# Kernel optimization log

Measured on AMD Instinct MI355X. Metric: run time of the kernel, lower is better.

## Reference

```python
import jax, jax.numpy as jnp
import numpy as np

B, S, D_IN, D_OUT = 4, 2048, 1024, 1024
USE_MASK = True


def setup_inputs() -> dict:
    key = jax.random.key(0)
    ks = jax.random.split(key, 6)
    return {
        "inputs_for_keys": jax.random.normal(ks[0], (B, S, D_IN), jnp.float32),
        "inputs_for_values": jax.random.normal(ks[1], (B, S, D_IN), jnp.float32),
        "inputs_for_queries": jax.random.normal(ks[2], (B, S, D_IN), jnp.float32),
        "WK": jax.random.normal(ks[3], (D_IN, D_OUT), jnp.float32) * 0.1,
        "WV": jax.random.normal(ks[4], (D_IN, D_OUT), jnp.float32) * 0.1,
        "WQ": jax.random.normal(ks[5], (D_IN, D_OUT), jnp.float32) * 0.1,
    }


def reference(inputs_for_keys, inputs_for_values, inputs_for_queries, WK, WV, WQ):
    # projections: [B,S,Din] @ [Din,Dout] -> [B,S,Dout]
    K = jnp.einsum("bsd,de->bse", inputs_for_keys, WK)
    V = jnp.einsum("bsd,de->bse", inputs_for_values, WV)
    Q = jnp.einsum("bsd,de->bse", inputs_for_queries, WQ)

    dk = jnp.asarray(K.shape[2], jnp.float32)
    # scores: [B, Sq, Sk]
    score = jnp.einsum("bqd,bkd->bqk", Q, K) / jnp.sqrt(dk)
    if USE_MASK:
        # causal: -inf strictly above diagonal (j > i), matching the
        # transposed tril(-1) * -inf construction in the original.
        q_idx = jnp.arange(S)[:, None]
        k_idx = jnp.arange(S)[None, :]
        mask = jnp.where(k_idx > q_idx, -jnp.inf, 0.0).astype(score.dtype)
        score = score + mask[None, :, :]
    soft_score = jax.nn.softmax(score, axis=-1)
    return jnp.einsum("bqk,bkd->bqd", soft_score, V)
```

## Files before the change

### kernel.cpp

```cpp
#include <hip/hip_runtime.h>
#include <hip/hip_bf16.h>

typedef unsigned short u16;
typedef _Float16 f16;
typedef __attribute__((ext_vector_type(8))) short s16x8;
typedef __attribute__((ext_vector_type(8))) _Float16 f16x8;
typedef __attribute__((ext_vector_type(4))) float f32x4;
typedef __attribute__((ext_vector_type(4))) unsigned short u16x4;

template <typename T>
__device__ __forceinline__ auto mfma_try(T a, T b, f32x4 c, int)
    -> decltype(__builtin_amdgcn_mfma_f32_16x16x32_f16(a, b, c, 0, 0, 0)) {
  return __builtin_amdgcn_mfma_f32_16x16x32_f16(a, b, c, 0, 0, 0);
}
template <typename T>
__device__ __forceinline__ f32x4 mfma_try(T a, T b, f32x4 c, long) {
  return __builtin_amdgcn_mfma_f32_16x16x32_f16(
      __builtin_bit_cast(f16x8, a), __builtin_bit_cast(f16x8, b), c, 0, 0, 0);
}
__device__ __forceinline__ f32x4 MFMA16(s16x8 a, s16x8 b, f32x4 c) {
  return mfma_try(a, b, c, 0);
}

__device__ __forceinline__ void gload16(const void* g, void* s) {
  __builtin_amdgcn_global_load_lds(
      (const __attribute__((address_space(1))) void*)g,
      (__attribute__((address_space(3))) void*)s, 16, 0, 0);
}

__device__ __forceinline__ u16 f2h(float x) {
  f16 h = (f16)x;
  u16 u;
  __builtin_memcpy(&u, &h, 2);
  return u;
}
__device__ __forceinline__ float h2f(u16 u) {
  f16 h;
  __builtin_memcpy(&h, &u, 2);
  return (float)h;
}

#define LDS_SWZ(r, cb) ((cb) ^ (((r)&7) << 4))

__device__ __forceinline__ void bar() { __builtin_amdgcn_s_barrier(); }
__device__ __forceinline__ void lgkm0() {
  asm volatile("s_waitcnt lgkmcnt(0)" ::: "memory");
  __builtin_amdgcn_sched_barrier(0);
}
__device__ __forceinline__ void vm4() {
  asm volatile("s_waitcnt vmcnt(4)" ::: "memory");
}
__device__ __forceinline__ void vm0() {
  asm volatile("s_waitcnt vmcnt(0)" ::: "memory");
}

__device__ __forceinline__ void gemm256_core(
    const u16* __restrict__ Apan, int lda, const u16* __restrict__ Bpan,
    int ldb, int ns, char* lds, f32x4 (&acc)[8][4]) {
  const int tid = threadIdx.x;
  const int w = tid >> 6, l = tid & 63;
  const int wr = w >> 2, wc = w & 3;

  const int sr = tid >> 3;
  const int scol = (((tid & 7) * 16) ^ ((sr & 7) << 4)) >> 1;

  auto stageH = [&](const u16* pan, int ld, int t, int h, int region) {
    char* dst = lds + ((t & 1) << 16) + region * 16384 + (w << 10);
    const u16* src = pan + (long)(h * 128 + sr) * ld + t * 64 + scol;
    gload16(src, dst);
    gload16(src + (long)64 * ld, dst + 8192);
  };
  auto rdA = [&](int p, int m, int ks) -> s16x8 {
    int r = m * 16 + (l & 15);
    int cb = ks * 64 + ((l >> 4) << 4);
    return *(const s16x8*)(lds + (p << 16) + wr * 16384 + r * 128 + LDS_SWZ(r, cb));
  };
  auto rdB = [&](int p, int n, int ks) -> s16x8 {
    int row = wc * 64 + n * 16 + (l & 15);
    int r = row & 127;
    int cb = ks * 64 + ((l >> 4) << 4);
    return *(const s16x8*)(lds + (p << 16) + (2 + (wc >> 1)) * 16384 + r * 128 +
                           LDS_SWZ(r, cb));
  };

  stageH(Apan, lda, 0, 0, 0);
  stageH(Apan, lda, 0, 1, 1);
  stageH(Bpan, ldb, 0, 0, 2);
  stageH(Bpan, ldb, 0, 1, 3);
  if (ns > 1) {
    stageH(Apan, lda, 1, 0, 0);
    stageH(Apan, lda, 1, 1, 1);
    vm4();
  } else {
    vm0();
  }
  bar();

  for (int t = 0; t < ns; ++t) {
    const int p = t & 1;
    s16x8 af[8][2], bf[4][2];
    auto do_mfma = [&](int mb) {
#pragma unroll
      for (int m = 0; m < 2; ++m)
#pragma unroll
        for (int n = 0; n < 4; ++n) {
          acc[mb + m][n] = MFMA16(af[mb + m][0], bf[n][0], acc[mb + m][n]);
          acc[mb + m][n] = MFMA16(af[mb + m][1], bf[n][1], acc[mb + m][n]);
        }
    };
#pragma unroll
    for (int n = 0; n < 4; ++n) { bf[n][0] = rdB(p, n, 0); bf[n][1] = rdB(p, n, 1); }
#pragma unroll
    for (int m = 0; m < 2; ++m) { af[m][0] = rdA(p, m, 0); af[m][1] = rdA(p, m, 1); }
    if (t + 1 < ns) stageH(Bpan, ldb, t + 1, 0, 2);
    bar(); lgkm0();
    __builtin_amdgcn_s_setprio(1);
    do_mfma(0);
    __builtin_amdgcn_s_setprio(0);
    bar();
#pragma unroll
    for (int m = 2; m < 8; ++m) { af[m][0] = rdA(p, m, 0); af[m][1] = rdA(p, m, 1); }
    if (t + 1 < ns) stageH(Bpan, ldb, t + 1, 1, 3);
    bar(); lgkm0();
    __builtin_amdgcn_s_setprio(1);
    do_mfma(2);
    __builtin_amdgcn_s_setprio(0);
    bar();
    if (t + 2 < ns) stageH(Apan, lda, t + 2, 0, 0);
    bar(); lgkm0();
    __builtin_amdgcn_s_setprio(1);
    do_mfma(4);
    __builtin_amdgcn_s_setprio(0);
    bar();
    if (t + 2 < ns) stageH(Apan, lda, t + 2, 1, 1);
    bar(); lgkm0();
    __builtin_amdgcn_s_setprio(1);
    do_mfma(6);
    __builtin_amdgcn_s_setprio(0);
    if (t + 2 < ns) vm4(); else vm0();
    bar();
  }
}

__global__ __launch_bounds__(512, 2) void proj256_kernel(
    const u16* __restrict__ xk, const u16* __restrict__ xq, const u16* __restrict__ xv,
    const u16* __restrict__ wk, const u16* __restrict__ wq, const u16* __restrict__ wv,
    u16* __restrict__ K, u16* __restrict__ Q, u16* __restrict__ Vt) {
  __shared__ char lds[131072];
  const int y = blockIdx.y;
  const u16* X = y == 0 ? xk : (y == 1 ? xq : xv);
  const u16* W = y == 0 ? wk : (y == 1 ? wq : wv);
  const int bx = blockIdx.x;
  const int swz = (bx & 7) * 16 + (bx >> 3);
  const int tm = swz >> 2, tn = swz & 3;
  f32x4 acc[8][4] = {};
  gemm256_core(X + (long)tm * 256 * 1024, 1024, W + (long)tn * 256 * 1024, 1024,
               16, lds, acc);
  const int l = threadIdx.x & 63, w = threadIdx.x >> 6;
  const int wr = w >> 2, wc = w & 3;
  const int rg0 = tm * 256 + wr * 128, cg0 = tn * 256 + wc * 64;
  if (y < 2) {
    u16* C = y == 0 ? K : Q;
#pragma unroll
    for (int m = 0; m < 8; ++m)
#pragma unroll
      for (int n = 0; n < 4; ++n)
#pragma unroll
        for (int j = 0; j < 4; ++j) {
          int rg = rg0 + m * 16 + ((l >> 4) << 2) + j;
          int cg = cg0 + n * 16 + (l & 15);
          C[(long)rg * 1024 + cg] = f2h(acc[m][n][j]);
        }
  } else {
#pragma unroll
    for (int m = 0; m < 8; ++m) {
      int rg = rg0 + m * 16 + ((l >> 4) << 2);
      int b = rg >> 11, rl = rg & 2047;
#pragma unroll
      for (int n = 0; n < 4; ++n) {
        int cg = cg0 + n * 16 + (l & 15);
        u16x4 pk;
#pragma unroll
        for (int j = 0; j < 4; ++j) pk[j] = f2h(acc[m][n][j]);
        *(u16x4*)(Vt + (long)b * (1024 * 2048) + (long)cg * 2048 + rl) = pk;
      }
    }
  }
}

__global__ __launch_bounds__(512, 2) void qkt256_kernel(
    const u16* __restrict__ Q, const u16* __restrict__ K, u16* __restrict__ S) {
  __shared__ char lds[131072];
  const int bx = blockIdx.x;
  const int swz = (bx & 7) * 18 + (bx >> 3);
  const int b = swz / 36;
  int t = swz - b * 36;
  int tm = 0;
  while (t > tm) { t -= tm + 1; ++tm; }
  const int tn = t;
  f32x4 acc[8][4] = {};
  const u16* Qb = Q + (long)b * 2048 * 1024;
  const u16* Kb = K + (long)b * 2048 * 1024;
  gemm256_core(Qb + (long)tm * 256 * 1024, 1024, Kb + (long)tn * 256 * 1024,
               1024, 16, lds, acc);
  u16* Sb = S + (long)b * 2048 * 2048;
  const int l = threadIdx.x & 63, w = threadIdx.x >> 6;
  const int wr = w >> 2, wc = w & 3;
  const int rg0 = tm * 256 + wr * 128, cg0 = tn * 256 + wc * 64;
#pragma unroll
  for (int m = 0; m < 8; ++m)
#pragma unroll
    for (int n = 0; n < 4; ++n)
#pragma unroll
      for (int j = 0; j < 4; ++j) {
        int rg = rg0 + m * 16 + ((l >> 4) << 2) + j;
        int cg = cg0 + n * 16 + (l & 15);
        Sb[(long)rg * 2048 + cg] = f2h(acc[m][n][j]);
      }
}

struct Geom {
  int srow[4], scol[4];
  int w, l, wr, wc;
};

__device__ __forceinline__ Geom make_geom() {
  Geom g;
  int tid = threadIdx.x;
  g.w = tid >> 6; g.l = tid & 63;
  g.wr = g.w >> 1; g.wc = g.w & 1;
#pragma unroll
  for (int i = 0; i < 4; ++i) {
    int off = i * 4096 + g.w * 1024 + g.l * 16;
    int r = off >> 7, cb = off & 127;
    g.srow[i] = r;
    g.scol[i] = LDS_SWZ(r, cb) >> 1;
  }
  return g;
}

__device__ __forceinline__ void stage(const u16* pan, int ld, int k0,
                                      char* lds, const Geom& g) {
#pragma unroll
  for (int i = 0; i < 4; ++i)
    gload16(pan + (long)g.srow[i] * ld + k0 + g.scol[i],
            lds + i * 4096 + g.w * 1024);
}

__device__ __forceinline__ void compute_step(const char* lA, const char* lB,
                                             const Geom& g, f32x4 acc[4][4]) {
#pragma unroll
  for (int ks = 0; ks < 2; ++ks) {
    s16x8 af[4], bg[4];
#pragma unroll
    for (int m = 0; m < 4; ++m) {
      int r = g.wr * 64 + m * 16 + (g.l & 15);
      int cb = ks * 64 + ((g.l >> 4) << 4);
      af[m] = *(const s16x8*)(lA + r * 128 + LDS_SWZ(r, cb));
    }
#pragma unroll
    for (int n = 0; n < 4; ++n) {
      int r = g.wc * 64 + n * 16 + (g.l & 15);
      int cb = ks * 64 + ((g.l >> 4) << 4);
      bg[n] = *(const s16x8*)(lB + r * 128 + LDS_SWZ(r, cb));
    }
#pragma unroll
    for (int m = 0; m < 4; ++m)
#pragma unroll
      for (int n = 0; n < 4; ++n)
        acc[m][n] = MFMA16(af[m], bg[n], acc[m][n]);
  }
}

__device__ __forceinline__ void gemm_core(const u16* Apan, int lda,
                                          const u16* Bpan, int ldb, int nsteps,
                                          char* lA, char* lB, const Geom& g,
                                          f32x4 acc[4][4]) {
  stage(Apan, lda, 0, lA, g);
  stage(Bpan, ldb, 0, lB, g);
  __syncthreads();
  for (int t = 0; t < nsteps; ++t) {
    int cur = (t & 1) << 14;
    if (t + 1 < nsteps) {
      int nxt = ((t + 1) & 1) << 14;
      stage(Apan, lda, (t + 1) * 64, lA + nxt, g);
      stage(Bpan, ldb, (t + 1) * 64, lB + nxt, g);
    }
    compute_step(lA + cur, lB + cur, g, acc);
    if (t + 1 < nsteps) __syncthreads();
  }
}

__global__ __launch_bounds__(256, 2) void pv_kernel(
    const u16* __restrict__ P, const u16* __restrict__ Vt, float* __restrict__ O) {
  __shared__ char lds[65536];
  const int bx = blockIdx.x;
  const int swz = (bx & 7) * 64 + (bx >> 3);
  const int b = swz >> 7, loc = swz & 127;
  const int tm = loc >> 3, tn = loc & 7;
  Geom g = make_geom();
  f32x4 acc[4][4] = {};
  gemm_core(P + ((long)b * 2048 + tm * 128) * 2048, 2048,
            Vt + (long)b * 1024 * 2048 + (long)tn * 128 * 2048, 2048,
            (tm + 1) * 2, lds, lds + 32768, g, acc);
  const int rg0 = tm * 128 + g.wr * 64, cg0 = tn * 128 + g.wc * 64;
#pragma unroll
  for (int m = 0; m < 4; ++m)
#pragma unroll
    for (int n = 0; n < 4; ++n)
#pragma unroll
      for (int j = 0; j < 4; ++j) {
        int rg = rg0 + m * 16 + ((g.l >> 4) << 2) + j;
        int cg = cg0 + n * 16 + (g.l & 15);
        O[((long)b * 2048 + rg) * 1024 + cg] = acc[m][n][j];
      }
}

__global__ __launch_bounds__(256) void softmax_causal(
    const u16* __restrict__ S, u16* __restrict__ P) {
  const int row = blockIdx.x;
  const int i_q = row & 2047;
  const u16* sr = S + (long)row * 2048;
  u16* pr = P + (long)row * 2048;
  const int tid = threadIdx.x;
  const int l = tid & 63, w = tid >> 6;
  const int base = tid * 8;

  s16x8 raw = *(const s16x8*)(sr + base);
  float v[8];
  float m = -INFINITY;
#pragma unroll
  for (int j = 0; j < 8; ++j) {
    float x = h2f((u16)raw[j]);
    x = (base + j <= i_q) ? x : -INFINITY;
    v[j] = x;
    m = fmaxf(m, x);
  }
  __shared__ float red[8];
  for (int o = 32; o; o >>= 1) m = fmaxf(m, __shfl_xor(m, o, 64));
  if (l == 0) red[w] = m;
  __syncthreads();
  m = fmaxf(fmaxf(red[0], red[1]), fmaxf(red[2], red[3]));

  float s = 0.f;
#pragma unroll
  for (int j = 0; j < 8; ++j) {
    v[j] = expf(v[j] - m);
    s += v[j];
  }
  for (int o = 32; o; o >>= 1) s += __shfl_xor(s, o, 64);
  if (l == 0) red[4 + w] = s;
  __syncthreads();
  s = (red[4] + red[5]) + (red[6] + red[7]);
  float inv = 1.0f / s;

  s16x8 o;
#pragma unroll
  for (int j = 0; j < 8; ++j) o[j] = (short)f2h(v[j] * inv);
  *(s16x8*)(pr + base) = o;
}

__global__ __launch_bounds__(256) void xcast_kernel(
    const float* __restrict__ x0, const float* __restrict__ x1,
    const float* __restrict__ x2, u16* __restrict__ o0, u16* __restrict__ o1,
    u16* __restrict__ o2) {
  const int y = blockIdx.y;
  const float* in = y == 0 ? x0 : (y == 1 ? x1 : x2);
  u16* out = y == 0 ? o0 : (y == 1 ? o1 : o2);
  long i = ((long)blockIdx.x * 256 + threadIdx.x) * 8;
  f32x4 a = *(const f32x4*)(in + i);
  f32x4 b = *(const f32x4*)(in + i + 4);
  s16x8 o;
#pragma unroll
  for (int j = 0; j < 4; ++j) {
    o[j] = (short)f2h(a[j]);
    o[4 + j] = (short)f2h(b[j]);
  }
  *(s16x8*)(out + i) = o;
}

__global__ __launch_bounds__(256) void wcast_kernel(
    const float* __restrict__ wk, const float* __restrict__ wv,
    const float* __restrict__ wq, u16* __restrict__ ok, u16* __restrict__ ov,
    u16* __restrict__ oq) {
  __shared__ float tile[32][33];
  const int z = blockIdx.z;
  const float* w = z == 0 ? wk : (z == 1 ? wv : wq);
  u16* o = z == 0 ? ok : (z == 1 ? ov : oq);
  const float scale = (z == 2) ? 0.03125f : 1.0f;
  const int bx = blockIdx.x, by = blockIdx.y;
  const int lx = threadIdx.x & 31, ly = threadIdx.x >> 5;
#pragma unroll
  for (int j = 0; j < 32; j += 8)
    tile[ly + j][lx] = w[(long)(by * 32 + ly + j) * 1024 + bx * 32 + lx];
  __syncthreads();
#pragma unroll
  for (int j = 0; j < 32; j += 8)
    o[(long)(bx * 32 + ly + j) * 1024 + by * 32 + lx] = f2h(tile[lx][ly + j] * scale);
}

extern "C" void kernel_launch(void* const* d_in, const int* in_sizes, int n_in,
                              void* d_out, int out_size, void* d_ws, size_t ws_size,
                              hipStream_t stream) {
  const float* Xk = (const float*)d_in[0];
  const float* Xv = (const float*)d_in[1];
  const float* Xq = (const float*)d_in[2];
  const float* WK = (const float*)d_in[3];
  const float* WV = (const float*)d_in[4];
  const float* WQ = (const float*)d_in[5];

  const int Bn = 4, S = 2048, D = 1024;
  const long NX = (long)Bn * S * D;

  const size_t r0 = (size_t)Bn * S * S * 4;
  const size_t r1 = r0 + 3ull * D * D * 2;
  const size_t r2 = r1 + 2ull * NX * 2;
  const size_t NEED = r2 + (size_t)NX * 2;
  if (ws_size < NEED) {
    hipMemsetAsync(d_out, 0, (size_t)out_size * 4, stream);
    return;
  }
  char* ws = (char*)d_ws;
  u16* xkb = (u16*)ws;
  u16* xvb = xkb + NX;
  u16* xqb = xvb + NX;
  u16* scoresH = (u16*)ws;
  u16* wkt = (u16*)(ws + r0);
  u16* wvt = wkt + D * D;
  u16* wqt = wvt + D * D;
  u16* Kb = (u16*)(ws + r1);
  u16* Qb = Kb + NX;
  u16* Pb = (u16*)(ws + r1);
  u16* Vt = (u16*)(ws + r2);

  xcast_kernel<<<dim3(4096, 3), 256, 0, stream>>>(Xk, Xv, Xq, xkb, xvb, xqb);
  wcast_kernel<<<dim3(32, 32, 3), 256, 0, stream>>>(WK, WV, WQ, wkt, wvt, wqt);
  proj256_kernel<<<dim3(128, 3), 512, 0, stream>>>(xkb, xqb, xvb, wkt, wqt, wvt,
                                                   Kb, Qb, Vt);
  qkt256_kernel<<<dim3(144), 512, 0, stream>>>(Qb, Kb, scoresH);
  softmax_causal<<<dim3(8192), 256, 0, stream>>>(scoresH, Pb);
  pv_kernel<<<dim3(512), 256, 0, stream>>>(Pb, Vt, (float*)d_out);
}
```

Before: 171.7 us.

## Rework 256-tile GEMM pipeline into full double buffering; use 128-tile QK^T kernel

The 256x256 projection GEMM core is restructured into a templated k_step that double-buffers both A and B panels two steps ahead. It issues A and B loads together, with partial lgkm/vmcnt waits, so global loads overlap more MFMA work. The QK^T kernel is replaced by a 128x128-tile version built on the existing gemm_core, launching 544 lower-triangular blocks instead of 144. This gives better CU occupancy and load balance on the causal scores. The cost is more redundant panel loads in QK^T and more complex wait-count bookkeeping in the projection.

```diff
diff --git a/kernel.cpp b/kernel.cpp
--- a/kernel.cpp
+++ b/kernel.cpp
@@ -47,98 +47,100 @@
   asm volatile("s_waitcnt lgkmcnt(0)" ::: "memory");
   __builtin_amdgcn_sched_barrier(0);
 }
-__device__ __forceinline__ void vm4() {
-  asm volatile("s_waitcnt vmcnt(4)" ::: "memory");
-}
-__device__ __forceinline__ void vm0() {
-  asm volatile("s_waitcnt vmcnt(0)" ::: "memory");
-}
-
-__device__ __forceinline__ void gemm256_core(
+
+template <int P>
+__device__ __forceinline__ void k_step(
     const u16* __restrict__ Apan, int lda, const u16* __restrict__ Bpan,
-    int ldb, int ns, char* lds, f32x4 (&acc)[8][4]) {
+    int ldb, int t, int NS, char* lds, int l, int w, int wr, int wc, int sr,
+    int scol, f32x4 (&acc)[8][4]) {
+  constexpr int BUF = P << 16;
+  s16x8 af[8][2], bf[4][2];
+  auto rdA = [&](int m, int ks) -> s16x8 {
+    int r = m * 16 + (l & 15);
+    int cb = ks * 64 + ((l >> 4) << 4);
+    return *(const s16x8*)(lds + BUF + wr * 16384 + r * 128 + LDS_SWZ(r, cb));
+  };
+  auto rdB = [&](int n, int ks) -> s16x8 {
+    int row = wc * 64 + n * 16 + (l & 15);
+    int r = row & 127;
+    int cb = ks * 64 + ((l >> 4) << 4);
+    return *(const s16x8*)(lds + BUF + 32768 + (wc >> 1) * 16384 + r * 128 +
+                           LDS_SWZ(r, cb));
+  };
+  auto stageH = [&](const u16* pan, int ld, int tt, int h, int region) {
+    char* dst = lds + BUF + region * 16384 + (w << 10);
+    const u16* src = pan + (long)(h * 128 + sr) * ld + tt * 64 + scol;
+    gload16(src, dst);
+    gload16(src + (long)64 * ld, dst + 8192);
+  };
+  auto mfma2 = [&](int mb) {
+#pragma unroll
+    for (int m = mb; m < mb + 2; ++m)
+#pragma unroll
+      for (int n = 0; n < 4; ++n) {
+        acc[m][n] = MFMA16(af[m][0], bf[n][0], acc[m][n]);
+        acc[m][n] = MFMA16(af[m][1], bf[n][1], acc[m][n]);
+      }
+  };
+#pragma unroll
+  for (int n = 0; n < 4; ++n) { bf[n][0] = rdB(n, 0); bf[n][1] = rdB(n, 1); }
+#pragma unroll
+  for (int m = 0; m < 2; ++m) { af[m][0] = rdA(m, 0); af[m][1] = rdA(m, 1); }
+  asm volatile("s_waitcnt lgkmcnt(8)" ::: "memory");
+  bar(); lgkm0();
+  __builtin_amdgcn_s_setprio(1); mfma2(0); __builtin_amdgcn_s_setprio(0);
+  bar();
+#pragma unroll
+  for (int m = 2; m < 8; ++m) { af[m][0] = rdA(m, 0); af[m][1] = rdA(m, 1); }
+  asm volatile("s_waitcnt lgkmcnt(8)" ::: "memory");
+  bar(); lgkm0();
+  __builtin_amdgcn_s_setprio(1); mfma2(2); __builtin_amdgcn_s_setprio(0);
+  bar();
+  if (t + 2 < NS) {
+    stageH(Apan, lda, t + 2, 0, 0);
+    stageH(Bpan, ldb, t + 2, 0, 2);
+  }
+  bar();
+  __builtin_amdgcn_s_setprio(1); mfma2(4); __builtin_amdgcn_s_setprio(0);
+  bar();
+  if (t + 2 < NS) {
+    stageH(Apan, lda, t + 2, 1, 1);
+    stageH(Bpan, ldb, t + 2, 1, 3);
+    asm volatile("s_waitcnt vmcnt(8)" ::: "memory");
+  } else {
+    asm volatile("s_waitcnt vmcnt(0)" ::: "memory");
+  }
+  bar();
+  __builtin_amdgcn_s_setprio(1); mfma2(6); __builtin_amdgcn_s_setprio(0);
+  bar();
+}
+
+__device__ __forceinline__ void gemm256_core(const u16* __restrict__ Apan,
+                                             int lda,
+                                             const u16* __restrict__ Bpan,
+                                             int ldb, char* lds,
+                                             f32x4 (&acc)[8][4]) {
   const int tid = threadIdx.x;
   const int w = tid >> 6, l = tid & 63;
   const int wr = w >> 2, wc = w & 3;
-
   const int sr = tid >> 3;
   const int scol = (((tid & 7) * 16) ^ ((sr & 7) << 4)) >> 1;
-
-  auto stageH = [&](const u16* pan, int ld, int t, int h, int region) {
+  constexpr int NS = 16;
+  auto stageP = [&](const u16* pan, int ld, int t, int h, int region) {
     char* dst = lds + ((t & 1) << 16) + region * 16384 + (w << 10);
     const u16* src = pan + (long)(h * 128 + sr) * ld + t * 64 + scol;
     gload16(src, dst);
     gload16(src + (long)64 * ld, dst + 8192);
   };
-  auto rdA = [&](int p, int m, int ks) -> s16x8 {
-    int r = m * 16 + (l & 15);
-    int cb = ks * 64 + ((l >> 4) << 4);
-    return *(const s16x8*)(lds + (p << 16) + wr * 16384 + r * 128 + LDS_SWZ(r, cb));
-  };
-  auto rdB = [&](int p, int n, int ks) -> s16x8 {
-    int row = wc * 64 + n * 16 + (l & 15);
-    int r = row & 127;
-    int cb = ks * 64 + ((l >> 4) << 4);
-    return *(const s16x8*)(lds + (p << 16) + (2 + (wc >> 1)) * 16384 + r * 128 +
-                           LDS_SWZ(r, cb));
-  };
-
-  stageH(Apan, lda, 0, 0, 0);
-  stageH(Apan, lda, 0, 1, 1);
-  stageH(Bpan, ldb, 0, 0, 2);
-  stageH(Bpan, ldb, 0, 1, 3);
-  if (ns > 1) {
-    stageH(Apan, lda, 1, 0, 0);
-    stageH(Apan, lda, 1, 1, 1);
-    vm4();
-  } else {
-    vm0();
-  }
-  bar();
-
-  for (int t = 0; t < ns; ++t) {
-    const int p = t & 1;
-    s16x8 af[8][2], bf[4][2];
-    auto do_mfma = [&](int mb) {
-#pragma unroll
-      for (int m = 0; m < 2; ++m)
-#pragma unroll
-        for (int n = 0; n < 4; ++n) {
-          acc[mb + m][n] = MFMA16(af[mb + m][0], bf[n][0], acc[mb + m][n]);
-          acc[mb + m][n] = MFMA16(af[mb + m][1], bf[n][1], acc[mb + m][n]);
-        }
-    };
-#pragma unroll
-    for (int n = 0; n < 4; ++n) { bf[n][0] = rdB(p, n, 0); bf[n][1] = rdB(p, n, 1); }
-#pragma unroll
-    for (int m = 0; m < 2; ++m) { af[m][0] = rdA(p, m, 0); af[m][1] = rdA(p, m, 1); }
-    if (t + 1 < ns) stageH(Bpan, ldb, t + 1, 0, 2);
-    bar(); lgkm0();
-    __builtin_amdgcn_s_setprio(1);
-    do_mfma(0);
-    __builtin_amdgcn_s_setprio(0);
-    bar();
-#pragma unroll
-    for (int m = 2; m < 8; ++m) { af[m][0] = rdA(p, m, 0); af[m][1] = rdA(p, m, 1); }
-    if (t + 1 < ns) stageH(Bpan, ldb, t + 1, 1, 3);
-    bar(); lgkm0();
-    __builtin_amdgcn_s_setprio(1);
-    do_mfma(2);
-    __builtin_amdgcn_s_setprio(0);
-    bar();
-    if (t + 2 < ns) stageH(Apan, lda, t + 2, 0, 0);
-    bar(); lgkm0();
-    __builtin_amdgcn_s_setprio(1);
-    do_mfma(4);
-    __builtin_amdgcn_s_setprio(0);
-    bar();
-    if (t + 2 < ns) stageH(Apan, lda, t + 2, 1, 1);
-    bar(); lgkm0();
-    __builtin_amdgcn_s_setprio(1);
-    do_mfma(6);
-    __builtin_amdgcn_s_setprio(0);
-    if (t + 2 < ns) vm4(); else vm0();
-    bar();
+  stageP(Apan, lda, 0, 0, 0); stageP(Apan, lda, 0, 1, 1);
+  stageP(Bpan, ldb, 0, 0, 2); stageP(Bpan, ldb, 0, 1, 3);
+  stageP(Apan, lda, 1, 0, 0); stageP(Apan, lda, 1, 1, 1);
+  stageP(Bpan, ldb, 1, 0, 2); stageP(Bpan, ldb, 1, 1, 3);
+  asm volatile("s_waitcnt vmcnt(8)" ::: "memory");
+  bar();
+  for (int t = 0; t < NS; t += 2) {
+    k_step<0>(Apan, lda, Bpan, ldb, t, NS, lds, l, w, wr, wc, sr, scol, acc);
+    k_step<1>(Apan, lda, Bpan, ldb, t + 1, NS, lds, l, w, wr, wc, sr, scol, acc);
   }
 }
 
@@ -155,7 +157,7 @@
   const int tm = swz >> 2, tn = swz & 3;
   f32x4 acc[8][4] = {};
   gemm256_core(X + (long)tm * 256 * 1024, 1024, W + (long)tn * 256 * 1024, 1024,
-               16, lds, acc);
+               lds, acc);
   const int l = threadIdx.x & 63, w = threadIdx.x >> 6;
   const int wr = w >> 2, wc = w & 3;
   const int rg0 = tm * 256 + wr * 128, cg0 = tn * 256 + wc * 64;
@@ -186,37 +188,6 @@
       }
     }
   }
-}
-
-__global__ __launch_bounds__(512, 2) void qkt256_kernel(
-    const u16* __restrict__ Q, const u16* __restrict__ K, u16* __restrict__ S) {
-  __shared__ char lds[131072];
-  const int bx = blockIdx.x;
-  const int swz = (bx & 7) * 18 + (bx >> 3);
-  const int b = swz / 36;
-  int t = swz - b * 36;
-  int tm = 0;
-  while (t > tm) { t -= tm + 1; ++tm; }
-  const int tn = t;
-  f32x4 acc[8][4] = {};
-  const u16* Qb = Q + (long)b * 2048 * 1024;
-  const u16* Kb = K + (long)b * 2048 * 1024;
-  gemm256_core(Qb + (long)tm * 256 * 1024, 1024, Kb + (long)tn * 256 * 1024,
-               1024, 16, lds, acc);
-  u16* Sb = S + (long)b * 2048 * 2048;
-  const int l = threadIdx.x & 63, w = threadIdx.x >> 6;
-  const int wr = w >> 2, wc = w & 3;
-  const int rg0 = tm * 256 + wr * 128, cg0 = tn * 256 + wc * 64;
-#pragma unroll
-  for (int m = 0; m < 8; ++m)
-#pragma unroll
-    for (int n = 0; n < 4; ++n)
-#pragma unroll
-      for (int j = 0; j < 4; ++j) {
-        int rg = rg0 + m * 16 + ((l >> 4) << 2) + j;
-        int cg = cg0 + n * 16 + (l & 15);
-        Sb[(long)rg * 2048 + cg] = f2h(acc[m][n][j]);
-      }
 }
 
 struct Geom {
@@ -291,6 +262,36 @@
   }
 }
 
+__global__ __launch_bounds__(256, 2) void qkt_kernel(
+    const u16* __restrict__ Q, const u16* __restrict__ K, u16* __restrict__ S) {
+  __shared__ char lds[65536];
+  const int bx = blockIdx.x;
+  const int swz = (bx & 7) * 68 + (bx >> 3);
+  const int b = swz / 136;
+  int t = swz - b * 136;
+  int tm = 0;
+  while (t > tm) { t -= tm + 1; ++tm; }
+  const int tn = t;
+  Geom g = make_geom();
+  f32x4 acc[4][4] = {};
+  const u16* Qb = Q + (long)b * 2048 * 1024;
+  const u16* Kb = K + (long)b * 2048 * 1024;
+  gemm_core(Qb + (long)tm * 128 * 1024, 1024, Kb + (long)tn * 128 * 1024, 1024,
+            16, lds, lds + 32768, g, acc);
+  u16* Sb = S + (long)b * 2048 * 2048;
+  const int rg0 = tm * 128 + g.wr * 64, cg0 = tn * 128 + g.wc * 64;
+#pragma unroll
+  for (int m = 0; m < 4; ++m)
+#pragma unroll
+    for (int n = 0; n < 4; ++n)
+#pragma unroll
+      for (int j = 0; j < 4; ++j) {
+        int rg = rg0 + m * 16 + ((g.l >> 4) << 2) + j;
+        int cg = cg0 + n * 16 + (g.l & 15);
+        Sb[(long)rg * 2048 + cg] = f2h(acc[m][n][j]);
+      }
+}
+
 __global__ __launch_bounds__(256, 2) void pv_kernel(
     const u16* __restrict__ P, const u16* __restrict__ Vt, float* __restrict__ O) {
   __shared__ char lds[65536];
@@ -437,7 +438,7 @@
   wcast_kernel<<<dim3(32, 32, 3), 256, 0, stream>>>(WK, WV, WQ, wkt, wvt, wqt);
   proj256_kernel<<<dim3(128, 3), 512, 0, stream>>>(xkb, xqb, xvb, wkt, wqt, wvt,
                                                    Kb, Qb, Vt);
-  qkt256_kernel<<<dim3(144), 512, 0, stream>>>(Qb, Kb, scoresH);
+  qkt_kernel<<<dim3(544), 256, 0, stream>>>(Qb, Kb, scoresH);
   softmax_causal<<<dim3(8192), 256, 0, stream>>>(scoresH, Pb);
   pv_kernel<<<dim3(512), 256, 0, stream>>>(Pb, Vt, (float*)d_out);
 }
```

Result: no change. 175.1 us (+1.9%).
